# Kernel optimization log

Measured on AMD Instinct MI355X. Metric: run time of the kernel, lower is better.

The kernel has to match this reference:

```python
import jax, jax.numpy as jnp
import numpy as np

B, D, V = 2048, 512, 50304


def setup_inputs() -> dict:
    key = jax.random.key(0)
    ks = jax.random.split(key, 7)
    scale = 1.0 / np.sqrt(D)
    return {
        "student_h": jax.random.normal(ks[0], (B, D), dtype=jnp.float32) * scale,
        "student_c": jax.random.normal(ks[1], (V, D), dtype=jnp.float32) * scale,
        "teacher_h": jax.random.normal(ks[2], (B, D), dtype=jnp.float32) * scale,
        "teacher_c": jax.random.normal(ks[3], (V, D), dtype=jnp.float32) * scale,
        "ce_coeff": jax.random.uniform(ks[4], (B,), dtype=jnp.float32),
        "kl_coeff": jax.random.uniform(ks[5], (B,), dtype=jnp.float32),
        "targets": jax.random.randint(ks[6], (B,), 0, V, dtype=jnp.int64),
    }


def reference(student_h, student_c, teacher_h, teacher_c, ce_coeff, kl_coeff, targets):
    # Fused linear head: student/teacher logits over the full vocab  [B, V]
    s_logits = jnp.einsum("bd,vd->bv", student_h, student_c)
    t_logits = jnp.einsum("bd,vd->bv", teacher_h, teacher_c)

    s_lse = jax.nn.logsumexp(s_logits, axis=1)  # [B]
    t_lse = jax.nn.logsumexp(t_logits, axis=1)  # [B]

    # Cross-entropy per row: lse - logit[target]
    tgt_logit = jnp.take_along_axis(s_logits, targets[:, None], axis=1)[:, 0]
    ce = s_lse - tgt_logit  # [B]

    # KL(teacher || student) per row
    log_ps = s_logits - s_lse[:, None]
    log_pt = t_logits - t_lse[:, None]
    pt = jnp.exp(log_pt)
    kl = jnp.sum(pt * (log_pt - log_ps), axis=1)  # [B]

    # Per-row coefficients absorb any reduction weighting (as in the kernel)
    loss = jnp.sum(ce_coeff * ce + kl_coeff * kl)
    return loss
```

## Files before the change

kernel.cpp:

```cpp
#include <hip/hip_runtime.h>
#include <hip/hip_fp8.h>

#define B_ 2048
#define D_ 512
#define V_ 50304
#define NROWB 16
#define NCOLB 393
#define NWG (NROWB * NCOLB)
#define NCOPY 32
#define LOG2E 1.44269504088896340736f
#define LN2 0.69314718055994530942f

typedef __attribute__((ext_vector_type(4))) float f32x4;
typedef __attribute__((ext_vector_type(2))) unsigned long ulx2;
typedef __attribute__((ext_vector_type(8))) int v8i;
typedef unsigned char u8;

__device__ inline void gload16(const void* g, void* l) {
  __builtin_amdgcn_global_load_lds((const __attribute__((address_space(1))) void*)g,
                                   (__attribute__((address_space(3))) void*)l, 16, 0, 0);
}

__global__ void cast8t_kernel(const float* __restrict__ src, uint4* __restrict__ dst,
                              float scale, int nchunk) {
  int i = blockIdx.x * blockDim.x + threadIdx.x;
  if (i >= nchunk) return;
  int c = i & 127;
  int j = (i >> 7) & 7;
  int kk = (i >> 10) & 3;
  int p = i >> 12;
  const float4* s = (const float4*)(src + (size_t)(p * 128 + c) * 512 + kk * 128 + j * 16);
  union { u8 b[16]; uint4 u; } o;
#pragma unroll
  for (int q = 0; q < 4; ++q) {
    float4 f = s[q];
    o.b[q * 4 + 0] = __hip_fp8_e4m3(f.x * scale).__x;
    o.b[q * 4 + 1] = __hip_fp8_e4m3(f.y * scale).__x;
    o.b[q * 4 + 2] = __hip_fp8_e4m3(f.z * scale).__x;
    o.b[q * 4 + 3] = __hip_fp8_e4m3(f.w * scale).__x;
  }
  dst[i] = o.u;
}

__global__ void cast8_kernel(const float* __restrict__ src, uint2* __restrict__ dst,
                             float scale, int n8) {
  int i = blockIdx.x * blockDim.x + threadIdx.x;
  int stride = gridDim.x * blockDim.x;
  const float4* s4 = (const float4*)src;
  for (; i < n8; i += stride) {
    float4 a = s4[2 * i], b = s4[2 * i + 1];
    union { u8 c[8]; uint2 u; } p;
    p.c[0] = __hip_fp8_e4m3(a.x * scale).__x;
    p.c[1] = __hip_fp8_e4m3(a.y * scale).__x;
    p.c[2] = __hip_fp8_e4m3(a.z * scale).__x;
    p.c[3] = __hip_fp8_e4m3(a.w * scale).__x;
    p.c[4] = __hip_fp8_e4m3(b.x * scale).__x;
    p.c[5] = __hip_fp8_e4m3(b.y * scale).__x;
    p.c[6] = __hip_fp8_e4m3(b.z * scale).__x;
    p.c[7] = __hip_fp8_e4m3(b.w * scale).__x;
    dst[i] = p.u;
  }
}

__global__ void tgt_kernel(const float* __restrict__ sh, const float* __restrict__ sc,
                           const int* __restrict__ targets, float* __restrict__ tgt_out) {
  int gid = blockIdx.x * blockDim.x + threadIdx.x;
  int w = gid >> 6, lane = gid & 63;
  if (w >= B_) return;
  int tgt = targets[w];
  const float4* a = (const float4*)(sh + (size_t)w * D_);
  const float4* b = (const float4*)(sc + (size_t)tgt * D_);
  float acc = 0.f;
#pragma unroll
  for (int i = 0; i < 2; ++i) {
    float4 x = a[lane + i * 64], y = b[lane + i * 64];
    acc += x.x * y.x + x.y * y.y + x.z * y.z + x.w * y.w;
  }
#pragma unroll
  for (int off = 1; off < 64; off <<= 1) acc += __shfl_xor(acc, off);
  if (lane == 0) tgt_out[w] = acc;
}

__global__ __launch_bounds__(256, 2) void lce_main(
    const u8* __restrict__ SH8, const u8* __restrict__ TH8,
    const u8* __restrict__ SC8t, const u8* __restrict__ TC8t,
    float* __restrict__ stats32) {
  __shared__ __align__(16) u8 smem[2][2][16384];

  const int tid = threadIdx.x;
  const int lane = tid & 63, w = tid >> 6;
  const int mat = w & 1;
  const int wr = w >> 1;
  const int rA = lane & 15;
  const int kg = lane >> 4;

  int hw = blockIdx.x;
  int lid = (hw & 7) * 786 + (hw >> 3);
  const int row0 = (lid & 15) * 128;
  const int p = lid >> 4;
  const int jcopy = (hw & 7) * 4 + ((lid >> 4) & 3);
  float* stats = stats32 + (size_t)jcopy * B_ * 3;

  const u8* gB[2] = {SC8t + (size_t)p * 65536 + tid * 16,
                     TC8t + (size_t)p * 65536 + tid * 16};

  const u8* gA = (mat ? TH8 : SH8) + (size_t)(row0 + wr * 64 + rA) * D_ + kg * 32;

  f32x4 acc[4][8];
#pragma unroll
  for (int i = 0; i < 4; ++i)
#pragma unroll
    for (int j = 0; j < 8; ++j) acc[i][j] = (f32x4){0.f, 0.f, 0.f, 0.f};

  v8i av[2][4];

#define STAGE(buf, kk)                                                        \
  {                                                                           \
    _Pragma("unroll") for (int mt = 0; mt < 2; ++mt) {                        \
      _Pragma("unroll") for (int r = 0; r < 4; ++r) {                         \
        gload16(gB[mt] + (kk) * 16384 + r * 4096,                             \
                &smem[buf][mt][r * 4096 + tid * 16]);                         \
      }                                                                       \
    }                                                                         \
  }

#define LOADA(buf, kk)                                                        \
  {                                                                           \
    _Pragma("unroll") for (int mi = 0; mi < 4; ++mi) {                        \
      av[buf][mi] = *(const v8i*)(gA + (size_t)(mi * 16) * D_ + (kk) * 128);  \
    }                                                                         \
  }

  STAGE(0, 0);
  LOADA(0, 0);

#pragma unroll
  for (int kk = 0; kk < 4; ++kk) {
    const int par = kk & 1;
    if (kk < 3) {
      STAGE(par ^ 1, kk + 1);
      LOADA(par ^ 1, kk + 1);
    }
    if (kk < 3)
      asm volatile("s_waitcnt vmcnt(16)\n\ts_barrier" ::: "memory");
    else
      asm volatile("s_waitcnt vmcnt(8)\n\ts_barrier" ::: "memory");

    __builtin_amdgcn_s_setprio(1);
#pragma unroll
    for (int ni = 0; ni < 8; ++ni) {
      const u8* bp = &smem[par][mat][(2 * kg) * 2048 + (ni * 16 + rA) * 16];
      union { struct { ulx2 lo, hi; } s; v8i v; } ub;
      ub.s.lo = *(const ulx2*)bp;
      ub.s.hi = *(const ulx2*)(bp + 2048);
#pragma unroll
      for (int mi = 0; mi < 4; ++mi)
        acc[mi][ni] = __builtin_amdgcn_mfma_scale_f32_16x16x128_f8f6f4(
            av[par][mi], ub.v, acc[mi][ni], 0, 0, 0, 127, 0, 127);
    }
    __builtin_amdgcn_s_setprio(0);
    asm volatile("s_barrier" ::: "memory");
  }

  const float inv = 1.0f / 256.0f;
  float2* exch = (float2*)smem;

  if (mat == 0) {
#pragma unroll
    for (int mi = 0; mi < 4; ++mi)
#pragma unroll
      for (int ni = 0; ni < 8; ++ni)
#pragma unroll
        for (int rp = 0; rp < 2; ++rp) {
          float2 v = make_float2(acc[mi][ni][2 * rp] * inv, acc[mi][ni][2 * rp + 1] * inv);
          exch[(size_t)((((wr * 4 + mi) * 8 + ni) * 2 + rp) * 64 + lane)] = v;
        }
  }
  asm volatile("s_waitcnt lgkmcnt(0)\n\ts_barrier" ::: "memory");

  if (mat == 0) {
#pragma unroll
    for (int mi = 0; mi < 4; ++mi) {
      float ssr[4] = {0.f, 0.f, 0.f, 0.f};
#pragma unroll
      for (int ni = 0; ni < 8; ++ni)
#pragma unroll
        for (int reg = 0; reg < 4; ++reg)
          ssr[reg] += __builtin_amdgcn_exp2f(acc[mi][ni][reg] * inv);
#pragma unroll
      for (int reg = 0; reg < 4; ++reg) {
        float v = ssr[reg];
#pragma unroll
        for (int off = 1; off < 16; off <<= 1) v += __shfl_xor(v, off);
        if (rA == 0)
          atomicAdd(&stats[(size_t)(row0 + wr * 64 + mi * 16 + kg * 4 + reg) * 3 + 0], v);
      }
    }
  } else {
#pragma unroll
    for (int mi = 0; mi < 4; ++mi) {
      float str[4] = {0.f, 0.f, 0.f, 0.f};
      float atr[4] = {0.f, 0.f, 0.f, 0.f};
#pragma unroll
      for (int ni = 0; ni < 8; ++ni)
#pragma unroll
        for (int rp = 0; rp < 2; ++rp) {
          float2 sv = exch[(size_t)((((wr * 4 + mi) * 8 + ni) * 2 + rp) * 64 + lane)];
          float tv0 = acc[mi][ni][2 * rp] * inv;
          float tv1 = acc[mi][ni][2 * rp + 1] * inv;
          float et0 = __builtin_amdgcn_exp2f(tv0);
          float et1 = __builtin_amdgcn_exp2f(tv1);
          str[2 * rp] += et0;
          str[2 * rp + 1] += et1;
          atr[2 * rp] += et0 * (tv0 - sv.x);
          atr[2 * rp + 1] += et1 * (tv1 - sv.y);
        }
#pragma unroll
      for (int reg = 0; reg < 4; ++reg) {
        float v = str[reg], u = atr[reg];
#pragma unroll
        for (int off = 1; off < 16; off <<= 1) {
          v += __shfl_xor(v, off);
          u += __shfl_xor(u, off);
        }
        if (rA == 0) {
          size_t r = (size_t)(row0 + wr * 64 + mi * 16 + kg * 4 + reg) * 3;
          atomicAdd(&stats[r + 1], v);
          atomicAdd(&stats[r + 2], u);
        }
      }
    }
  }
}

__global__ void finalize(const float* __restrict__ stats32, const float* __restrict__ tgt,
                         const float* __restrict__ cec, const float* __restrict__ klc,
                         float* __restrict__ out) {
  __shared__ float red[16];
  int tid = threadIdx.x;
  float acc = 0.f;
  for (int r = tid; r < B_; r += 1024) {
    float ss = 0.f, st = 0.f, at = 0.f;
#pragma unroll
    for (int j = 0; j < NCOPY; ++j) {
      const float* s = stats32 + ((size_t)j * B_ + r) * 3;
      ss += s[0]; st += s[1]; at += s[2];
    }
    float s_lse = LN2 * __builtin_amdgcn_logf(ss);
    float t_lse = LN2 * __builtin_amdgcn_logf(st);
    float kl = s_lse - t_lse + LN2 * at / st;
    float ce = s_lse - tgt[r];
    acc += cec[r] * ce + klc[r] * kl;
  }
#pragma unroll
  for (int off = 1; off < 64; off <<= 1) acc += __shfl_xor(acc, off);
  if ((tid & 63) == 0) red[tid >> 6] = acc;
  __syncthreads();
  if (tid == 0) {
    float s = 0.f;
#pragma unroll
    for (int i = 0; i < 16; ++i) s += red[i];
    out[0] = s;
  }
}

extern "C" void kernel_launch(void* const* d_in, const int* in_sizes, int n_in,
                              void* d_out, int out_size, void* d_ws, size_t ws_size,
                              hipStream_t stream) {
  const float* sh = (const float*)d_in[0];
  const float* sc = (const float*)d_in[1];
  const float* th = (const float*)d_in[2];
  const float* tc = (const float*)d_in[3];
  const float* cec = (const float*)d_in[4];
  const float* klc = (const float*)d_in[5];
  const int* targets = (const int*)d_in[6];
  float* out = (float*)d_out;

  char* ws = (char*)d_ws;
  u8* SC8t = (u8*)ws;
  u8* TC8t = SC8t + (size_t)V_ * D_;
  u8* SH8 = TC8t + (size_t)V_ * D_;
  u8* TH8 = SH8 + (size_t)B_ * D_;
  float* stats32 = (float*)(TH8 + (size_t)B_ * D_);
  float* tgt = stats32 + (size_t)NCOPY * B_ * 3;

  hipMemsetAsync(stats32, 0, (size_t)NCOPY * B_ * 3 * sizeof(float), stream);
  const float hscale = 16.0f * LOG2E;
  const float cscale = 16.0f;
  const int nchunk = V_ * D_ / 16;
  cast8t_kernel<<<(nchunk + 255) / 256, 256, 0, stream>>>(sc, (uint4*)SC8t, cscale, nchunk);
  cast8t_kernel<<<(nchunk + 255) / 256, 256, 0, stream>>>(tc, (uint4*)TC8t, cscale, nchunk);
  cast8_kernel<<<256, 256, 0, stream>>>(sh, (uint2*)SH8, hscale, B_ * D_ / 8);
  cast8_kernel<<<256, 256, 0, stream>>>(th, (uint2*)TH8, hscale, B_ * D_ / 8);
  tgt_kernel<<<512, 256, 0, stream>>>(sh, sc, targets, tgt);

  lce_main<<<NWG, 256, 0, stream>>>(SH8, TH8, SC8t, TC8t, stats32);
  finalize<<<1, 1024, 0, stream>>>(stats32, tgt, cec, klc, out);
}
```

Before: 292.4 us.

## Process three vocab panels per workgroup with LDS stats and partial-sum output

After: 673.9 us. 130% more time.

```diff
diff --git a/kernel.cpp b/kernel.cpp
--- a/kernel.cpp
+++ b/kernel.cpp
@@ -4,9 +4,8 @@
 #define B_ 2048
 #define D_ 512
 #define V_ 50304
-#define NROWB 16
-#define NCOLB 393
-#define NWG (NROWB * NCOLB)
+#define NPG 131
+#define NWG (16 * NPG)
 #define NCOPY 32
 #define LOG2E 1.44269504088896340736f
 #define LN2 0.69314718055994530942f
@@ -19,6 +18,12 @@
 __device__ inline void gload16(const void* g, void* l) {
   __builtin_amdgcn_global_load_lds((const __attribute__((address_space(1))) void*)g,
                                    (__attribute__((address_space(3))) void*)l, 16, 0, 0);
+}
+
+__device__ inline unsigned f2bf(float f) {
+  unsigned u = __float_as_uint(f);
+  u += 0x7fffu + ((u >> 16) & 1u);
+  return u >> 16;
 }
 
 __global__ void cast8t_kernel(const float* __restrict__ src, uint4* __restrict__ dst,
@@ -81,11 +86,13 @@
   if (lane == 0) tgt_out[w] = acc;
 }
 
+template <bool PART>
 __global__ __launch_bounds__(256, 2) void lce_main(
     const u8* __restrict__ SH8, const u8* __restrict__ TH8,
     const u8* __restrict__ SC8t, const u8* __restrict__ TC8t,
-    float* __restrict__ stats32) {
+    float* __restrict__ gout) {
   __shared__ __align__(16) u8 smem[2][2][16384];
+  __shared__ float lstats[128][3];
 
   const int tid = threadIdx.x;
   const int lane = tid & 63, w = tid >> 6;
@@ -94,146 +101,166 @@
   const int rA = lane & 15;
   const int kg = lane >> 4;
 
-  int hw = blockIdx.x;
-  int lid = (hw & 7) * 786 + (hw >> 3);
+  const int hw = blockIdx.x;
+  const int lid = (hw & 7) * (NWG / 8) + (hw >> 3);
   const int row0 = (lid & 15) * 128;
-  const int p = lid >> 4;
-  const int jcopy = (hw & 7) * 4 + ((lid >> 4) & 3);
-  float* stats = stats32 + (size_t)jcopy * B_ * 3;
-
-  const u8* gB[2] = {SC8t + (size_t)p * 65536 + tid * 16,
-                     TC8t + (size_t)p * 65536 + tid * 16};
-
+  const int pg = lid >> 4;
+
+  if (tid < 128) { lstats[tid][0] = 0.f; lstats[tid][1] = 0.f; lstats[tid][2] = 0.f; }
+
+  const u8* gBs = SC8t + (size_t)(pg * 3) * 65536 + tid * 16;
+  const u8* gBt = TC8t + (size_t)(pg * 3) * 65536 + tid * 16;
   const u8* gA = (mat ? TH8 : SH8) + (size_t)(row0 + wr * 64 + rA) * D_ + kg * 32;
 
   f32x4 acc[4][8];
-#pragma unroll
-  for (int i = 0; i < 4; ++i)
-#pragma unroll
-    for (int j = 0; j < 8; ++j) acc[i][j] = (f32x4){0.f, 0.f, 0.f, 0.f};
-
   v8i av[2][4];
 
-#define STAGE(buf, kk)                                                        \
+#define STAGE(buf, pnl, kk)                                                   \
   {                                                                           \
-    _Pragma("unroll") for (int mt = 0; mt < 2; ++mt) {                        \
-      _Pragma("unroll") for (int r = 0; r < 4; ++r) {                         \
-        gload16(gB[mt] + (kk) * 16384 + r * 4096,                             \
-                &smem[buf][mt][r * 4096 + tid * 16]);                         \
-      }                                                                       \
-    }                                                                         \
+    _Pragma("unroll") for (int r = 0; r < 4; ++r)                             \
+        gload16(gBs + ((pnl) * 4 + (kk)) * 16384 + r * 4096,                  \
+                &smem[buf][0][r * 4096 + tid * 16]);                          \
+    _Pragma("unroll") for (int r = 0; r < 4; ++r)                             \
+        gload16(gBt + ((pnl) * 4 + (kk)) * 16384 + r * 4096,                  \
+                &smem[buf][1][r * 4096 + tid * 16]);                          \
   }
 
 #define LOADA(buf, kk)                                                        \
   {                                                                           \
-    _Pragma("unroll") for (int mi = 0; mi < 4; ++mi) {                        \
-      av[buf][mi] = *(const v8i*)(gA + (size_t)(mi * 16) * D_ + (kk) * 128);  \
-    }                                                                         \
-  }
-
-  STAGE(0, 0);
+    _Pragma("unroll") for (int mi = 0; mi < 4; ++mi)                          \
+        av[buf][mi] = *(const v8i*)(gA + (size_t)(mi * 16) * D_ + (kk) * 128);\
+  }
+
+  const float inv = 1.0f / 256.0f;
+  uint* exch = (uint*)&smem[1][0][0];
+
+  STAGE(0, 0, 0);
   LOADA(0, 0);
 
-#pragma unroll
-  for (int kk = 0; kk < 4; ++kk) {
-    const int par = kk & 1;
-    if (kk < 3) {
-      STAGE(par ^ 1, kk + 1);
-      LOADA(par ^ 1, kk + 1);
-    }
-    if (kk < 3)
-      asm volatile("s_waitcnt vmcnt(16)\n\ts_barrier" ::: "memory");
-    else
-      asm volatile("s_waitcnt vmcnt(8)\n\ts_barrier" ::: "memory");
-
-    __builtin_amdgcn_s_setprio(1);
-#pragma unroll
-    for (int ni = 0; ni < 8; ++ni) {
-      const u8* bp = &smem[par][mat][(2 * kg) * 2048 + (ni * 16 + rA) * 16];
-      union { struct { ulx2 lo, hi; } s; v8i v; } ub;
-      ub.s.lo = *(const ulx2*)bp;
-      ub.s.hi = *(const ulx2*)(bp + 2048);
+  for (int pp = 0; pp < 3; ++pp) {
+#pragma unroll
+    for (int i = 0; i < 4; ++i)
+#pragma unroll
+      for (int j = 0; j < 8; ++j) acc[i][j] = (f32x4){0.f, 0.f, 0.f, 0.f};
+
+#pragma unroll
+    for (int kk = 0; kk < 4; ++kk) {
+      const int par = kk & 1;
+      if (kk < 3) {
+        STAGE(par ^ 1, pp, kk + 1);
+        LOADA(par ^ 1, kk + 1);
+        asm volatile("s_waitcnt vmcnt(16)\n\ts_barrier" ::: "memory");
+      } else if (pp < 2) {
+        STAGE(0, pp + 1, 0);
+        LOADA(0, 0);
+        asm volatile("s_waitcnt vmcnt(16)\n\ts_barrier" ::: "memory");
+      } else {
+        asm volatile("s_waitcnt vmcnt(4)\n\ts_barrier" ::: "memory");
+      }
+
+      __builtin_amdgcn_s_setprio(1);
+#pragma unroll
+      for (int ni = 0; ni < 8; ++ni) {
+        const u8* bp = &smem[par][mat][(2 * kg) * 2048 + (ni * 16 + rA) * 16];
+        union { struct { ulx2 lo, hi; } s; v8i v; } ub;
+        ub.s.lo = *(const ulx2*)bp;
+        ub.s.hi = *(const ulx2*)(bp + 2048);
+#pragma unroll
+        for (int mi = 0; mi < 4; ++mi)
+          acc[mi][ni] = __builtin_amdgcn_mfma_scale_f32_16x16x128_f8f6f4(
+              av[par][mi], ub.v, acc[mi][ni], 0, 0, 0, 127, 0, 127);
+      }
+      __builtin_amdgcn_s_setprio(0);
+      asm volatile("s_barrier" ::: "memory");
+    }
+
+    if (mat == 0) {
 #pragma unroll
       for (int mi = 0; mi < 4; ++mi)
-        acc[mi][ni] = __builtin_amdgcn_mfma_scale_f32_16x16x128_f8f6f4(
-            av[par][mi], ub.v, acc[mi][ni], 0, 0, 0, 127, 0, 127);
-    }
-    __builtin_amdgcn_s_setprio(0);
-    asm volatile("s_barrier" ::: "memory");
-  }
-
-  const float inv = 1.0f / 256.0f;
-  float2* exch = (float2*)smem;
-
-  if (mat == 0) {
-#pragma unroll
-    for (int mi = 0; mi < 4; ++mi)
-#pragma unroll
-      for (int ni = 0; ni < 8; ++ni)
-#pragma unroll
-        for (int rp = 0; rp < 2; ++rp) {
-          float2 v = make_float2(acc[mi][ni][2 * rp] * inv, acc[mi][ni][2 * rp + 1] * inv);
-          exch[(size_t)((((wr * 4 + mi) * 8 + ni) * 2 + rp) * 64 + lane)] = v;
+#pragma unroll
+        for (int ni = 0; ni < 8; ++ni)
+#pragma unroll
+          for (int rp = 0; rp < 2; ++rp) {
+            uint u = f2bf(acc[mi][ni][2 * rp] * inv) |
+                     (f2bf(acc[mi][ni][2 * rp + 1] * inv) << 16);
+            exch[(((wr * 4 + mi) * 8 + ni) * 2 + rp) * 64 + lane] = u;
+          }
+    }
+    asm volatile("s_waitcnt lgkmcnt(0)\n\ts_barrier" ::: "memory");
+
+    if (mat == 0) {
+#pragma unroll
+      for (int mi = 0; mi < 4; ++mi) {
+        float ssr[4] = {0.f, 0.f, 0.f, 0.f};
+#pragma unroll
+        for (int ni = 0; ni < 8; ++ni)
+#pragma unroll
+          for (int reg = 0; reg < 4; ++reg)
+            ssr[reg] += __builtin_amdgcn_exp2f(acc[mi][ni][reg] * inv);
+#pragma unroll
+        for (int reg = 0; reg < 4; ++reg) {
+          float v = ssr[reg];
+#pragma unroll
+          for (int off = 1; off < 16; off <<= 1) v += __shfl_xor(v, off);
+          if (rA == 0) atomicAdd(&lstats[wr * 64 + mi * 16 + kg * 4 + reg][0], v);
         }
-  }
-  asm volatile("s_waitcnt lgkmcnt(0)\n\ts_barrier" ::: "memory");
-
-  if (mat == 0) {
-#pragma unroll
-    for (int mi = 0; mi < 4; ++mi) {
-      float ssr[4] = {0.f, 0.f, 0.f, 0.f};
-#pragma unroll
-      for (int ni = 0; ni < 8; ++ni)
-#pragma unroll
-        for (int reg = 0; reg < 4; ++reg)
-          ssr[reg] += __builtin_amdgcn_exp2f(acc[mi][ni][reg] * inv);
-#pragma unroll
-      for (int reg = 0; reg < 4; ++reg) {
-        float v = ssr[reg];
-#pragma unroll
-        for (int off = 1; off < 16; off <<= 1) v += __shfl_xor(v, off);
-        if (rA == 0)
-          atomicAdd(&stats[(size_t)(row0 + wr * 64 + mi * 16 + kg * 4 + reg) * 3 + 0], v);
-      }
-    }
-  } else {
-#pragma unroll
-    for (int mi = 0; mi < 4; ++mi) {
-      float str[4] = {0.f, 0.f, 0.f, 0.f};
-      float atr[4] = {0.f, 0.f, 0.f, 0.f};
-#pragma unroll
-      for (int ni = 0; ni < 8; ++ni)
-#pragma unroll
-        for (int rp = 0; rp < 2; ++rp) {
-          float2 sv = exch[(size_t)((((wr * 4 + mi) * 8 + ni) * 2 + rp) * 64 + lane)];
-          float tv0 = acc[mi][ni][2 * rp] * inv;
-          float tv1 = acc[mi][ni][2 * rp + 1] * inv;
-          float et0 = __builtin_amdgcn_exp2f(tv0);
-          float et1 = __builtin_amdgcn_exp2f(tv1);
-          str[2 * rp] += et0;
-          str[2 * rp + 1] += et1;
-          atr[2 * rp] += et0 * (tv0 - sv.x);
-          atr[2 * rp + 1] += et1 * (tv1 - sv.y);
+      }
+    } else {
+#pragma unroll
+      for (int mi = 0; mi < 4; ++mi) {
+        float str[4] = {0.f, 0.f, 0.f, 0.f};
+        float atr[4] = {0.f, 0.f, 0.f, 0.f};
+#pragma unroll
+        for (int ni = 0; ni < 8; ++ni)
+#pragma unroll
+          for (int rp = 0; rp < 2; ++rp) {
+            uint u = exch[(((wr * 4 + mi) * 8 + ni) * 2 + rp) * 64 + lane];
+            float sv0 = __uint_as_float(u << 16);
+            float sv1 = __uint_as_float(u & 0xffff0000u);
+            float tv0 = acc[mi][ni][2 * rp] * inv;
+            float tv1 = acc[mi][ni][2 * rp + 1] * inv;
+            float et0 = __builtin_amdgcn_exp2f(tv0);
+            float et1 = __builtin_amdgcn_exp2f(tv1);
+            str[2 * rp] += et0;
+            str[2 * rp + 1] += et1;
+            atr[2 * rp] += et0 * (tv0 - sv0);
+            atr[2 * rp + 1] += et1 * (tv1 - sv1);
+          }
+#pragma unroll
+        for (int reg = 0; reg < 4; ++reg) {
+          float v = str[reg], uu = atr[reg];
+#pragma unroll
+          for (int off = 1; off < 16; off <<= 1) {
+            v += __shfl_xor(v, off);
+            uu += __shfl_xor(uu, off);
+          }
+          if (rA == 0) {
+            int row = wr * 64 + mi * 16 + kg * 4 + reg;
+            atomicAdd(&lstats[row][1], v);
+            atomicAdd(&lstats[row][2], uu);
+          }
         }
-#pragma unroll
-      for (int reg = 0; reg < 4; ++reg) {
-        float v = str[reg], u = atr[reg];
-#pragma unroll
-        for (int off = 1; off < 16; off <<= 1) {
-          v += __shfl_xor(v, off);
-          u += __shfl_xor(u, off);
-        }
-        if (rA == 0) {
-          size_t r = (size_t)(row0 + wr * 64 + mi * 16 + kg * 4 + reg) * 3;
-          atomicAdd(&stats[r + 1], v);
-          atomicAdd(&stats[r + 2], u);
-        }
-      }
-    }
-  }
-}
-
-__global__ void finalize(const float* __restrict__ stats32, const float* __restrict__ tgt,
+      }
+    }
+    __syncthreads();
+  }
+
+  if (tid < 128) {
+    float ss = lstats[tid][0], st = lstats[tid][1], at = lstats[tid][2];
+    if (PART) {
+      ((float4*)gout)[(size_t)pg * B_ + row0 + tid] = make_float4(ss, st, at, 0.f);
+    } else {
+      const int jcopy = (hw & 7) * 4 + (pg & 3);
+      float* s = gout + ((size_t)jcopy * B_ + row0 + tid) * 3;
+      atomicAdd(s + 0, ss);
+      atomicAdd(s + 1, st);
+      atomicAdd(s + 2, at);
+    }
+  }
+}
+
+template <bool PART>
+__global__ void finalize(const float* __restrict__ gout, const float* __restrict__ tgt,
                          const float* __restrict__ cec, const float* __restrict__ klc,
                          float* __restrict__ out) {
   __shared__ float red[16];
@@ -241,10 +268,17 @@
   float acc = 0.f;
   for (int r = tid; r < B_; r += 1024) {
     float ss = 0.f, st = 0.f, at = 0.f;
-#pragma unroll
-    for (int j = 0; j < NCOPY; ++j) {
-      const float* s = stats32 + ((size_t)j * B_ + r) * 3;
-      ss += s[0]; st += s[1]; at += s[2];
+    if (PART) {
+      const float4* p = (const float4*)gout + r;
+      for (int pgi = 0; pgi < NPG; ++pgi) {
+        float4 v = p[(size_t)pgi * B_];
+        ss += v.x; st += v.y; at += v.z;
+      }
+    } else {
+      for (int j = 0; j < NCOPY; ++j) {
+        const float* s = gout + ((size_t)j * B_ + r) * 3;
+        ss += s[0]; st += s[1]; at += s[2];
+      }
     }
     float s_lse = LN2 * __builtin_amdgcn_logf(ss);
     float t_lse = LN2 * __builtin_amdgcn_logf(st);
@@ -281,10 +315,14 @@
   u8* TC8t = SC8t + (size_t)V_ * D_;
   u8* SH8 = TC8t + (size_t)V_ * D_;
   u8* TH8 = SH8 + (size_t)B_ * D_;
-  float* stats32 = (float*)(TH8 + (size_t)B_ * D_);
-  float* tgt = stats32 + (size_t)NCOPY * B_ * 3;
-
-  hipMemsetAsync(stats32, 0, (size_t)NCOPY * B_ * 3 * sizeof(float), stream);
+  const size_t base = (size_t)2 * V_ * D_ + (size_t)2 * B_ * D_;
+  float* gout = (float*)(ws + base);
+  const size_t part_bytes = (size_t)NPG * B_ * 16;
+  const size_t fall_bytes = (size_t)NCOPY * B_ * 3 * 4;
+  bool part = ws_size >= base + part_bytes + 8192;
+  float* tgt = (float*)(ws + base + (part ? part_bytes : fall_bytes));
+
+  if (!part) hipMemsetAsync(gout, 0, fall_bytes, stream);
   const float hscale = 16.0f * LOG2E;
   const float cscale = 16.0f;
   const int nchunk = V_ * D_ / 16;
@@ -294,6 +332,11 @@
   cast8_kernel<<<256, 256, 0, stream>>>(th, (uint2*)TH8, hscale, B_ * D_ / 8);
   tgt_kernel<<<512, 256, 0, stream>>>(sh, sc, targets, tgt);
 
-  lce_main<<<NWG, 256, 0, stream>>>(SH8, TH8, SC8t, TC8t, stats32);
-  finalize<<<1, 1024, 0, stream>>>(stats32, tgt, cec, klc, out);
-}
+  if (part) {
+    lce_main<true><<<NWG, 256, 0, stream>>>(SH8, TH8, SC8t, TC8t, gout);
+    finalize<true><<<1, 1024, 0, stream>>>(gout, tgt, cec, klc, out);
+  } else {
+    lce_main<false><<<NWG, 256, 0, stream>>>(SH8, TH8, SC8t, TC8t, gout);
+    finalize<false><<<1, 1024, 0, stream>>>(gout, tgt, cec, klc, out);
+  }
+}
```

## Load B fragments directly from global and shrink exchange buffer to bf16

Applied to the files above, without the earlier changes.

Result: no change. 293.1 us (+0.2%).

```diff
diff --git a/kernel.cpp b/kernel.cpp
--- a/kernel.cpp
+++ b/kernel.cpp
@@ -12,13 +12,13 @@
 #define LN2 0.69314718055994530942f
 
 typedef __attribute__((ext_vector_type(4))) float f32x4;
-typedef __attribute__((ext_vector_type(2))) unsigned long ulx2;
 typedef __attribute__((ext_vector_type(8))) int v8i;
 typedef unsigned char u8;
 
-__device__ inline void gload16(const void* g, void* l) {
-  __builtin_amdgcn_global_load_lds((const __attribute__((address_space(1))) void*)g,
-                                   (__attribute__((address_space(3))) void*)l, 16, 0, 0);
+__device__ inline unsigned f2bf(float f) {
+  unsigned u = __float_as_uint(f);
+  u += 0x7fffu + ((u >> 16) & 1u);
+  return u >> 16;
 }
 
 __global__ void cast8t_kernel(const float* __restrict__ src, uint4* __restrict__ dst,
@@ -26,20 +26,21 @@
   int i = blockIdx.x * blockDim.x + threadIdx.x;
   if (i >= nchunk) return;
   int c = i & 127;
-  int j = (i >> 7) & 7;
-  int kk = (i >> 10) & 3;
-  int p = i >> 12;
-  const float4* s = (const float4*)(src + (size_t)(p * 128 + c) * 512 + kk * 128 + j * 16);
-  union { u8 b[16]; uint4 u; } o;
-#pragma unroll
-  for (int q = 0; q < 4; ++q) {
+  int jp = (i >> 7) & 3;
+  int kk = (i >> 9) & 3;
+  int p = i >> 11;
+  const float4* s = (const float4*)(src + (size_t)(p * 128 + c) * 512 + kk * 128 + jp * 32);
+  union { u8 b[32]; uint4 u[2]; } o;
+#pragma unroll
+  for (int q = 0; q < 8; ++q) {
     float4 f = s[q];
     o.b[q * 4 + 0] = __hip_fp8_e4m3(f.x * scale).__x;
     o.b[q * 4 + 1] = __hip_fp8_e4m3(f.y * scale).__x;
     o.b[q * 4 + 2] = __hip_fp8_e4m3(f.z * scale).__x;
     o.b[q * 4 + 3] = __hip_fp8_e4m3(f.w * scale).__x;
   }
-  dst[i] = o.u;
+  dst[2 * i] = o.u[0];
+  dst[2 * i + 1] = o.u[1];
 }
 
 __global__ void cast8_kernel(const float* __restrict__ src, uint2* __restrict__ dst,
@@ -85,7 +86,7 @@
     const u8* __restrict__ SH8, const u8* __restrict__ TH8,
     const u8* __restrict__ SC8t, const u8* __restrict__ TC8t,
     float* __restrict__ stats32) {
-  __shared__ __align__(16) u8 smem[2][2][16384];
+  __shared__ __align__(16) uint exch[8192];
 
   const int tid = threadIdx.x;
   const int lane = tid & 63, w = tid >> 6;
@@ -94,16 +95,14 @@
   const int rA = lane & 15;
   const int kg = lane >> 4;
 
-  int hw = blockIdx.x;
-  int lid = (hw & 7) * 786 + (hw >> 3);
+  const int hw = blockIdx.x;
+  const int lid = (hw & 7) * 786 + (hw >> 3);
   const int row0 = (lid & 15) * 128;
   const int p = lid >> 4;
   const int jcopy = (hw & 7) * 4 + ((lid >> 4) & 3);
   float* stats = stats32 + (size_t)jcopy * B_ * 3;
 
-  const u8* gB[2] = {SC8t + (size_t)p * 65536 + tid * 16,
-                     TC8t + (size_t)p * 65536 + tid * 16};
-
+  const u8* gB = (mat ? TC8t : SC8t) + (size_t)p * 65536 + kg * 4096 + rA * 32;
   const u8* gA = (mat ? TH8 : SH8) + (size_t)(row0 + wr * 64 + rA) * D_ + kg * 32;
 
   f32x4 acc[4][8];
@@ -112,58 +111,27 @@
 #pragma unroll
     for (int j = 0; j < 8; ++j) acc[i][j] = (f32x4){0.f, 0.f, 0.f, 0.f};
 
-  v8i av[2][4];
-
-#define STAGE(buf, kk)                                                        \
-  {                                                                           \
-    _Pragma("unroll") for (int mt = 0; mt < 2; ++mt) {                        \
-      _Pragma("unroll") for (int r = 0; r < 4; ++r) {                         \
-        gload16(gB[mt] + (kk) * 16384 + r * 4096,                             \
-                &smem[buf][mt][r * 4096 + tid * 16]);                         \
-      }                                                                       \
-    }                                                                         \
-  }
-
-#define LOADA(buf, kk)                                                        \
-  {                                                                           \
-    _Pragma("unroll") for (int mi = 0; mi < 4; ++mi) {                        \
-      av[buf][mi] = *(const v8i*)(gA + (size_t)(mi * 16) * D_ + (kk) * 128);  \
-    }                                                                         \
-  }
-
-  STAGE(0, 0);
-  LOADA(0, 0);
-
 #pragma unroll
   for (int kk = 0; kk < 4; ++kk) {
-    const int par = kk & 1;
-    if (kk < 3) {
-      STAGE(par ^ 1, kk + 1);
-      LOADA(par ^ 1, kk + 1);
-    }
-    if (kk < 3)
-      asm volatile("s_waitcnt vmcnt(16)\n\ts_barrier" ::: "memory");
-    else
-      asm volatile("s_waitcnt vmcnt(8)\n\ts_barrier" ::: "memory");
+    v8i av[4], bv[8];
+#pragma unroll
+    for (int mi = 0; mi < 4; ++mi)
+      av[mi] = *(const v8i*)(gA + (size_t)(mi * 16) * D_ + kk * 128);
+#pragma unroll
+    for (int ni = 0; ni < 8; ++ni)
+      bv[ni] = *(const v8i*)(gB + kk * 16384 + ni * 512);
 
     __builtin_amdgcn_s_setprio(1);
 #pragma unroll
-    for (int ni = 0; ni < 8; ++ni) {
-      const u8* bp = &smem[par][mat][(2 * kg) * 2048 + (ni * 16 + rA) * 16];
-      union { struct { ulx2 lo, hi; } s; v8i v; } ub;
-      ub.s.lo = *(const ulx2*)bp;
-      ub.s.hi = *(const ulx2*)(bp + 2048);
+    for (int ni = 0; ni < 8; ++ni)
 #pragma unroll
       for (int mi = 0; mi < 4; ++mi)
         acc[mi][ni] = __builtin_amdgcn_mfma_scale_f32_16x16x128_f8f6f4(
-            av[par][mi], ub.v, acc[mi][ni], 0, 0, 0, 127, 0, 127);
-    }
+            av[mi], bv[ni], acc[mi][ni], 0, 0, 0, 127, 0, 127);
     __builtin_amdgcn_s_setprio(0);
-    asm volatile("s_barrier" ::: "memory");
   }
 
   const float inv = 1.0f / 256.0f;
-  float2* exch = (float2*)smem;
 
   if (mat == 0) {
 #pragma unroll
@@ -172,8 +140,9 @@
       for (int ni = 0; ni < 8; ++ni)
 #pragma unroll
         for (int rp = 0; rp < 2; ++rp) {
-          float2 v = make_float2(acc[mi][ni][2 * rp] * inv, acc[mi][ni][2 * rp + 1] * inv);
-          exch[(size_t)((((wr * 4 + mi) * 8 + ni) * 2 + rp) * 64 + lane)] = v;
+          uint u = f2bf(acc[mi][ni][2 * rp] * inv) |
+                   (f2bf(acc[mi][ni][2 * rp + 1] * inv) << 16);
+          exch[(((wr * 4 + mi) * 8 + ni) * 2 + rp) * 64 + lane] = u;
         }
   }
   asm volatile("s_waitcnt lgkmcnt(0)\n\ts_barrier" ::: "memory");
@@ -205,15 +174,17 @@
       for (int ni = 0; ni < 8; ++ni)
 #pragma unroll
         for (int rp = 0; rp < 2; ++rp) {
-          float2 sv = exch[(size_t)((((wr * 4 + mi) * 8 + ni) * 2 + rp) * 64 + lane)];
+          uint u = exch[(((wr * 4 + mi) * 8 + ni) * 2 + rp) * 64 + lane];
+          float sv0 = __uint_as_float(u << 16);
+          float sv1 = __uint_as_float(u & 0xffff0000u);
           float tv0 = acc[mi][ni][2 * rp] * inv;
           float tv1 = acc[mi][ni][2 * rp + 1] * inv;
           float et0 = __builtin_amdgcn_exp2f(tv0);
           float et1 = __builtin_amdgcn_exp2f(tv1);
           str[2 * rp] += et0;
           str[2 * rp + 1] += et1;
-          atr[2 * rp] += et0 * (tv0 - sv.x);
-          atr[2 * rp + 1] += et1 * (tv1 - sv.y);
+          atr[2 * rp] += et0 * (tv0 - sv0);
+          atr[2 * rp + 1] += et1 * (tv1 - sv1);
         }
 #pragma unroll
       for (int reg = 0; reg < 4; ++reg) {
@@ -287,9 +258,9 @@
   hipMemsetAsync(stats32, 0, (size_t)NCOPY * B_ * 3 * sizeof(float), stream);
   const float hscale = 16.0f * LOG2E;
   const float cscale = 16.0f;
-  const int nchunk = V_ * D_ / 16;
-  cast8t_kernel<<<(nchunk + 255) / 256, 256, 0, stream>>>(sc, (uint4*)SC8t, cscale, nchunk);
-  cast8t_kernel<<<(nchunk + 255) / 256, 256, 0, stream>>>(tc, (uint4*)TC8t, cscale, nchunk);
+  const int nchunk = V_ * D_ / 32;
+  cast8t_kernel<<<3144, 256, 0, stream>>>(sc, (uint4*)SC8t, cscale, nchunk);
+  cast8t_kernel<<<3144, 256, 0, stream>>>(tc, (uint4*)TC8t, cscale, nchunk);
   cast8_kernel<<<256, 256, 0, stream>>>(sh, (uint2*)SH8, hscale, B_ * D_ / 8);
   cast8_kernel<<<256, 256, 0, stream>>>(th, (uint2*)TH8, hscale, B_ * D_ / 8);
   tgt_kernel<<<512, 256, 0, stream>>>(sh, sc, targets, tgt);
```

## Coalesce classifier fp8 cast via LDS transpose and split finalize reduction

Applied to the files above, without the earlier changes.

Result: faster. 272.6 us (-6.8%).

```diff
diff --git a/kernel.cpp b/kernel.cpp
--- a/kernel.cpp
+++ b/kernel.cpp
@@ -21,25 +21,48 @@
                                    (__attribute__((address_space(3))) void*)l, 16, 0, 0);
 }
 
-__global__ void cast8t_kernel(const float* __restrict__ src, uint4* __restrict__ dst,
-                              float scale, int nchunk) {
-  int i = blockIdx.x * blockDim.x + threadIdx.x;
-  if (i >= nchunk) return;
-  int c = i & 127;
-  int j = (i >> 7) & 7;
-  int kk = (i >> 10) & 3;
-  int p = i >> 12;
-  const float4* s = (const float4*)(src + (size_t)(p * 128 + c) * 512 + kk * 128 + j * 16);
-  union { u8 b[16]; uint4 u; } o;
-#pragma unroll
-  for (int q = 0; q < 4; ++q) {
-    float4 f = s[q];
-    o.b[q * 4 + 0] = __hip_fp8_e4m3(f.x * scale).__x;
-    o.b[q * 4 + 1] = __hip_fp8_e4m3(f.y * scale).__x;
-    o.b[q * 4 + 2] = __hip_fp8_e4m3(f.z * scale).__x;
-    o.b[q * 4 + 3] = __hip_fp8_e4m3(f.w * scale).__x;
-  }
-  dst[i] = o.u;
+__device__ inline unsigned f2bf(float f) {
+  unsigned u = __float_as_uint(f);
+  u += 0x7fffu + ((u >> 16) & 1u);
+  return u >> 16;
+}
+
+__global__ __launch_bounds__(256) void castT_kernel(const float* __restrict__ SC,
+                                                    const float* __restrict__ TC,
+                                                    u8* __restrict__ SC8t, u8* __restrict__ TC8t,
+                                                    float scale) {
+  __shared__ __align__(16) u8 lt[16384];
+  const int slab = blockIdx.x;
+  const int half = slab >= 1572;
+  const int s2 = half ? slab - 1572 : slab;
+  const int p = s2 >> 2, kk = s2 & 3;
+  const float* src = (half ? TC : SC) + (size_t)p * 128 * 512 + kk * 128;
+  u8* dst = (half ? TC8t : SC8t) + (size_t)s2 * 16384;
+
+  const int t = threadIdx.x;
+  const int rlo = t >> 5;
+  const int c16 = t & 31;
+  const int jslot = c16 >> 2, wi = c16 & 3;
+
+#pragma unroll
+  for (int i = 0; i < 16; ++i) {
+    const int row = i * 8 + rlo;
+    float4 f = *(const float4*)(src + (size_t)row * 512 + c16 * 4);
+    union { u8 b[4]; uint u; } o;
+    o.b[0] = __hip_fp8_e4m3(f.x * scale).__x;
+    o.b[1] = __hip_fp8_e4m3(f.y * scale).__x;
+    o.b[2] = __hip_fp8_e4m3(f.z * scale).__x;
+    o.b[3] = __hip_fp8_e4m3(f.w * scale).__x;
+    *(uint*)&lt[row * 128 + ((jslot ^ (row & 7)) * 16) + wi * 4] = o.u;
+  }
+  __syncthreads();
+#pragma unroll
+  for (int i = 0; i < 4; ++i) {
+    const int chunk = i * 256 + t;
+    const int js = chunk >> 7, c = chunk & 127;
+    uint4 v = *(const uint4*)&lt[c * 128 + ((js ^ (c & 7)) * 16)];
+    *(uint4*)(dst + js * 2048 + c * 16) = v;
+  }
 }
 
 __global__ void cast8_kernel(const float* __restrict__ src, uint2* __restrict__ dst,
@@ -101,9 +124,8 @@
   const int jcopy = (hw & 7) * 4 + ((lid >> 4) & 3);
   float* stats = stats32 + (size_t)jcopy * B_ * 3;
 
-  const u8* gB[2] = {SC8t + (size_t)p * 65536 + tid * 16,
-                     TC8t + (size_t)p * 65536 + tid * 16};
-
+  const u8* gBs = SC8t + (size_t)p * 65536 + tid * 16;
+  const u8* gBt = TC8t + (size_t)p * 65536 + tid * 16;
   const u8* gA = (mat ? TH8 : SH8) + (size_t)(row0 + wr * 64 + rA) * D_ + kg * 32;
 
   f32x4 acc[4][8];
@@ -118,7 +140,7 @@
   {                                                                           \
     _Pragma("unroll") for (int mt = 0; mt < 2; ++mt) {                        \
       _Pragma("unroll") for (int r = 0; r < 4; ++r) {                         \
-        gload16(gB[mt] + (kk) * 16384 + r * 4096,                             \
+        gload16((mt ? gBt : gBs) + (kk) * 16384 + r * 4096,                   \
                 &smem[buf][mt][r * 4096 + tid * 16]);                         \
       }                                                                       \
     }                                                                         \
@@ -233,35 +255,34 @@
   }
 }
 
-__global__ void finalize(const float* __restrict__ stats32, const float* __restrict__ tgt,
-                         const float* __restrict__ cec, const float* __restrict__ klc,
-                         float* __restrict__ out) {
-  __shared__ float red[16];
+__global__ void finalize1(const float* __restrict__ stats32, const float* __restrict__ tgt,
+                          const float* __restrict__ cec, const float* __restrict__ klc,
+                          float* __restrict__ rowvals) {
+  int r = blockIdx.x * blockDim.x + threadIdx.x;
+  if (r >= B_) return;
+  float ss = 0.f, st = 0.f, at = 0.f;
+#pragma unroll
+  for (int j = 0; j < NCOPY; ++j) {
+    const float* s = stats32 + ((size_t)j * B_ + r) * 3;
+    ss += s[0]; st += s[1]; at += s[2];
+  }
+  float s_lse = LN2 * __builtin_amdgcn_logf(ss);
+  float t_lse = LN2 * __builtin_amdgcn_logf(st);
+  float kl = s_lse - t_lse + LN2 * at / st;
+  float ce = s_lse - tgt[r];
+  rowvals[r] = cec[r] * ce + klc[r] * kl;
+}
+
+__global__ void finalize2(const float* __restrict__ rowvals, float* __restrict__ out) {
+  __shared__ float red[4];
   int tid = threadIdx.x;
-  float acc = 0.f;
-  for (int r = tid; r < B_; r += 1024) {
-    float ss = 0.f, st = 0.f, at = 0.f;
-#pragma unroll
-    for (int j = 0; j < NCOPY; ++j) {
-      const float* s = stats32 + ((size_t)j * B_ + r) * 3;
-      ss += s[0]; st += s[1]; at += s[2];
-    }
-    float s_lse = LN2 * __builtin_amdgcn_logf(ss);
-    float t_lse = LN2 * __builtin_amdgcn_logf(st);
-    float kl = s_lse - t_lse + LN2 * at / st;
-    float ce = s_lse - tgt[r];
-    acc += cec[r] * ce + klc[r] * kl;
-  }
-#pragma unroll
-  for (int off = 1; off < 64; off <<= 1) acc += __shfl_xor(acc, off);
-  if ((tid & 63) == 0) red[tid >> 6] = acc;
+  float a = 0.f;
+  for (int i = tid; i < B_; i += 256) a += rowvals[i];
+#pragma unroll
+  for (int off = 1; off < 64; off <<= 1) a += __shfl_xor(a, off);
+  if ((tid & 63) == 0) red[tid >> 6] = a;
   __syncthreads();
-  if (tid == 0) {
-    float s = 0.f;
-#pragma unroll
-    for (int i = 0; i < 16; ++i) s += red[i];
-    out[0] = s;
-  }
+  if (tid == 0) out[0] = red[0] + red[1] + red[2] + red[3];
 }
 
 extern "C" void kernel_launch(void* const* d_in, const int* in_sizes, int n_in,
@@ -283,17 +304,17 @@
   u8* TH8 = SH8 + (size_t)B_ * D_;
   float* stats32 = (float*)(TH8 + (size_t)B_ * D_);
   float* tgt = stats32 + (size_t)NCOPY * B_ * 3;
+  float* rowvals = tgt + B_;
 
   hipMemsetAsync(stats32, 0, (size_t)NCOPY * B_ * 3 * sizeof(float), stream);
   const float hscale = 16.0f * LOG2E;
   const float cscale = 16.0f;
-  const int nchunk = V_ * D_ / 16;
-  cast8t_kernel<<<(nchunk + 255) / 256, 256, 0, stream>>>(sc, (uint4*)SC8t, cscale, nchunk);
-  cast8t_kernel<<<(nchunk + 255) / 256, 256, 0, stream>>>(tc, (uint4*)TC8t, cscale, nchunk);
+  castT_kernel<<<2 * NCOLB * 4, 256, 0, stream>>>(sc, tc, SC8t, TC8t, cscale);
   cast8_kernel<<<256, 256, 0, stream>>>(sh, (uint2*)SH8, hscale, B_ * D_ / 8);
   cast8_kernel<<<256, 256, 0, stream>>>(th, (uint2*)TH8, hscale, B_ * D_ / 8);
   tgt_kernel<<<512, 256, 0, stream>>>(sh, sc, targets, tgt);
 
   lce_main<<<NWG, 256, 0, stream>>>(SH8, TH8, SC8t, TC8t, stats32);
-  finalize<<<1, 1024, 0, stream>>>(stats32, tgt, cec, klc, out);
-}
+  finalize1<<<16, 128, 0, stream>>>(stats32, tgt, cec, klc, rowvals);
+  finalize2<<<1, 256, 0, stream>>>(rowvals, out);
+}
```
